# Performance work log

Hardware: AMD Instinct MI355X
Metric: run time of the kernel (lower is better)

The kernel has to match this reference:

```python
import jax, jax.numpy as jnp
import numpy as np
import math

B, S, HID = 2, 2048, 1024
D = 64            # size_per_head
H = HID // D      # num heads = 16
ROT = 32          # rotary_hsize = size_per_head // 2


def _apply_rotary(qk, sinusoids):
    # qk: [B, S, H, D]; sinusoids: [B, 2, S, ROT]
    sin = sinusoids[:, 0, :, None, :]   # [B, S, 1, ROT]
    cos = sinusoids[:, 1, :, None, :]
    qk_rope = qk[..., :ROT]
    # torch.stack([-a[..., ::2], a[..., 1::2]], -1).reshape(a.shape)
    rot2 = jnp.stack([-qk_rope[..., ::2], qk_rope[..., 1::2]], axis=-1).reshape(qk_rope.shape)
    qk_rope = qk_rope * cos + rot2 * sin
    return jnp.concatenate([qk_rope, qk[..., ROT:]], axis=-1)


def setup_inputs() -> dict:
    key = jax.random.key(0)
    ks = jax.random.split(key, 8)
    sc = 1.0 / math.sqrt(HID)
    return {
        "x": jax.random.normal(ks[0], (B, S, HID), jnp.float32),
        "sinusoids": jax.random.normal(ks[1], (B, 2, S, ROT), jnp.float32),
        "attention_bias": jax.random.uniform(ks[2], (B, 1, S, S), jnp.float32),
        "Wq": jax.random.normal(ks[3], (HID, HID), jnp.float32) * sc,
        "bq": jnp.zeros((HID,), jnp.float32),
        "Wk": jax.random.normal(ks[4], (HID, HID), jnp.float32) * sc,
        "bk": jnp.zeros((HID,), jnp.float32),
        "Wv": jax.random.normal(ks[5], (HID, HID), jnp.float32) * sc,
        "bv": jnp.zeros((HID,), jnp.float32),
        "Wo": jax.random.normal(ks[6], (HID, HID), jnp.float32) * sc,
    }


def reference(x, sinusoids, attention_bias, Wq, bq, Wk, bk, Wv, bv, Wo):
    q = (x @ Wq + bq).reshape(B, S, H, D)
    k = (x @ Wk + bk).reshape(B, S, H, D)
    v = (x @ Wv + bv).reshape(B, S, H, D)
    # original concatenates q,k along the heads dim before rotary; since rotary
    # broadcasts over heads, applying it to each separately is identical math
    q = _apply_rotary(q, sinusoids)
    k = _apply_rotary(k, sinusoids)
    q = q / math.sqrt(D)
    scores = jnp.einsum('bqhd,bkhd->bhqk', q, k)          # [B,H,S,S]
    probs = jax.nn.softmax(scores, axis=-1)
    probs = probs * attention_bias                         # multiplicative bias AFTER softmax
    out = jnp.einsum('bhqk,bkhd->bqhd', probs, v)          # [B,S,H,D]
    out = out.reshape(B, S, HID)
    return out @ Wo
```

## Files before the change

kernel.cpp:

```cpp
#include <hip/hip_runtime.h>
#include <math.h>

#define B_   2
#define S_   2048
#define HID_ 1024
#define D_   64
#define H_   16
#define ROT_ 32
#define M_   (B_*S_)

typedef __attribute__((ext_vector_type(4))) short  short4v;
typedef __attribute__((ext_vector_type(8))) short  short8;
typedef __attribute__((ext_vector_type(4))) float  floatx4;
typedef __attribute__((ext_vector_type(16))) float floatx16;
typedef __attribute__((ext_vector_type(2))) unsigned int uint2v;

__device__ __forceinline__ unsigned short f2bf(float f) {
  unsigned int x = __builtin_bit_cast(unsigned int, f);
  x += 0x7fffu + ((x >> 16) & 1u);
  return (unsigned short)(x >> 16);
}
__device__ __forceinline__ unsigned int cvt_pk_bf16(float lo, float hi) {
  unsigned int r;
  asm("v_cvt_pk_bf16_f32 %0, %1, %2" : "=v"(r) : "v"(lo), "v"(hi));
  return r;
}
__device__ __forceinline__ void gload_lds16(const unsigned short* g, unsigned short* l) {
  __builtin_amdgcn_global_load_lds(
      (const __attribute__((address_space(1))) unsigned int*)g,
      (__attribute__((address_space(3))) unsigned int*)l, 16, 0, 0);
}

__global__ void cast_bf16(const float* __restrict__ in, unsigned short* __restrict__ out) {
  int i = (blockIdx.x * 256 + threadIdx.x) * 4;
  floatx4 v = *(const floatx4*)(in + i);
  unsigned short o[4];
  o[0] = f2bf(v[0]); o[1] = f2bf(v[1]); o[2] = f2bf(v[2]); o[3] = f2bf(v[3]);
  *(unsigned long long*)(out + i) = *(unsigned long long*)o;
}

__global__ void transW(const float* __restrict__ W0, const float* __restrict__ W1,
                       const float* __restrict__ W2, const float* __restrict__ W3,
                       unsigned short* __restrict__ T0, unsigned short* __restrict__ T1,
                       unsigned short* __restrict__ T2, unsigned short* __restrict__ T3) {
  const float* W; unsigned short* T;
  int z = blockIdx.z;
  if (z == 0)      { W = W0; T = T0; }
  else if (z == 1) { W = W1; T = T1; }
  else if (z == 2) { W = W2; T = T2; }
  else             { W = W3; T = T3; }
  __shared__ float tile[32][33];
  int bx = blockIdx.x * 32, by = blockIdx.y * 32;
  int tx = threadIdx.x, ty = threadIdx.y;
  #pragma unroll
  for (int j = 0; j < 4; j++)
    tile[ty + j*8][tx] = W[(size_t)(by + ty + j*8) * HID_ + bx + tx];
  __syncthreads();
  #pragma unroll
  for (int j = 0; j < 4; j++)
    T[(size_t)(bx + ty + j*8) * HID_ + by + tx] = f2bf(tile[tx][ty + j*8]);
}

template <int MODE>
__global__ __launch_bounds__(256) void gemm_bt(
    const unsigned short* __restrict__ A,
    const unsigned short* __restrict__ Bt0, const unsigned short* __restrict__ Bt1,
    const unsigned short* __restrict__ Bt2,
    const float* __restrict__ bias0, const float* __restrict__ bias1,
    const float* __restrict__ bias2,
    void* __restrict__ out0, void* __restrict__ out1, void* __restrict__ out2,
    const float* __restrict__ sins, float sc0)
{
  const unsigned short* Bt; const float* bias; void* Out; float sc;
  if (blockIdx.z == 0)      { Bt = Bt0; bias = bias0; Out = out0; sc = sc0; }
  else if (blockIdx.z == 1) { Bt = Bt1; bias = bias1; Out = out1; sc = 1.f; }
  else                      { Bt = Bt2; bias = bias2; Out = out2; sc = 1.f; }
  const int K = HID_, N = HID_;
  int m0 = blockIdx.y * 128, n0 = blockIdx.x * 128;
  __shared__ alignas(16) unsigned short sA[128 * 32];
  __shared__ alignas(16) unsigned short sB[128 * 32];
  int t = threadIdx.x;
  int lane = t & 63, wave = t >> 6;
  int quad = lane >> 4, l16 = lane & 15;
  int wr = wave >> 1, wc = wave & 1;

  int srow = (lane >> 2), scol = (lane & 3) * 8;
  const unsigned short* gA0 = A  + (size_t)(m0 + wave*32 +  0 + srow) * K + scol;
  const unsigned short* gA1 = A  + (size_t)(m0 + wave*32 + 16 + srow) * K + scol;
  const unsigned short* gB0 = Bt + (size_t)(n0 + wave*32 +  0 + srow) * K + scol;
  const unsigned short* gB1 = Bt + (size_t)(n0 + wave*32 + 16 + srow) * K + scol;
  unsigned short* lA0 = sA + (wave*32 +  0) * 32;
  unsigned short* lA1 = sA + (wave*32 + 16) * 32;
  unsigned short* lB0 = sB + (wave*32 +  0) * 32;
  unsigned short* lB1 = sB + (wave*32 + 16) * 32;

  floatx4 acc[4][4];
  #pragma unroll
  for (int i = 0; i < 4; i++)
    #pragma unroll
    for (int j = 0; j < 4; j++)
      acc[i][j] = (floatx4){0.f, 0.f, 0.f, 0.f};

  for (int k0 = 0; k0 < K; k0 += 32) {
    gload_lds16(gA0 + k0, lA0);
    gload_lds16(gA1 + k0, lA1);
    gload_lds16(gB0 + k0, lB0);
    gload_lds16(gB1 + k0, lB1);
    __syncthreads();
    short8 af[4], bf[4];
    #pragma unroll
    for (int i = 0; i < 4; i++) {
      af[i] = *(const short8*)(sA + (wr * 64 + i * 16 + l16) * 32 + quad * 8);
      bf[i] = *(const short8*)(sB + (wc * 64 + i * 16 + l16) * 32 + quad * 8);
    }
    #pragma unroll
    for (int i = 0; i < 4; i++)
      #pragma unroll
      for (int j = 0; j < 4; j++)
        acc[i][j] = __builtin_amdgcn_mfma_f32_16x16x32_bf16(af[i], bf[j], acc[i][j], 0, 0, 0);
    __syncthreads();
  }

  #pragma unroll
  for (int i = 0; i < 4; i++) {
    int mbase = m0 + wr * 64 + i * 16 + quad * 4;
    #pragma unroll
    for (int j = 0; j < 4; j++) {
      int n = n0 + wc * 64 + j * 16 + l16;
      float bv = bias ? bias[n] : 0.f;
      if (MODE == 1) {
        #pragma unroll
        for (int r = 0; r < 4; r++)
          ((float*)Out)[(size_t)(mbase + r) * N + n] = acc[i][j][r] + bv;
      } else if (blockIdx.z == 2) {
        int bb = mbase >> 11, ss = mbase & 2047;
        int hh = n >> 6, dd = n & 63;
        unsigned short pk[4];
        #pragma unroll
        for (int r = 0; r < 4; r++) pk[r] = f2bf(acc[i][j][r] + bv);
        *(unsigned long long*)((unsigned short*)Out +
            (((size_t)(bb * H_ + hh) * D_ + dd) * S_ + ss)) = *(unsigned long long*)pk;
      } else if (j < 2) {
        int jh = j * 16 + l16;
        #pragma unroll
        for (int r = 0; r < 4; r++) {
          int row = mbase + r, bb = row >> 11, ss = row & 2047;
          float sn = sins[((size_t)(bb * 2 + 0) * S_ + ss) * ROT_ + jh];
          float cs = sins[((size_t)(bb * 2 + 1) * S_ + ss) * ROT_ + jh];
          float f = (jh & 1) ? (cs + sn) : (cs - sn);
          ((unsigned short*)Out)[(size_t)row * N + n] = f2bf((acc[i][j][r] + bv) * f * sc);
        }
      } else {
        #pragma unroll
        for (int r = 0; r < 4; r++)
          ((unsigned short*)Out)[(size_t)(mbase + r) * N + n] = f2bf((acc[i][j][r] + bv) * sc);
      }
    }
  }
}

__global__ __launch_bounds__(256) void gemm_bt64(
    const unsigned short* __restrict__ A, const unsigned short* __restrict__ Bt,
    float* __restrict__ Out)
{
  const int K = HID_, N = HID_;
  int m0 = blockIdx.y * 128, n0 = blockIdx.x * 64;
  __shared__ alignas(16) unsigned short sA[128 * 32];
  __shared__ alignas(16) unsigned short sB[64 * 32];
  int t = threadIdx.x;
  int lane = t & 63, wave = t >> 6;
  int quad = lane >> 4, l16 = lane & 15;
  int wr = wave >> 1, wc = wave & 1;

  int srow = lane >> 2, scol = (lane & 3) * 8;
  const unsigned short* gA0 = A  + (size_t)(m0 + wave*32 +  0 + srow) * K + scol;
  const unsigned short* gA1 = A  + (size_t)(m0 + wave*32 + 16 + srow) * K + scol;
  const unsigned short* gB0 = Bt + (size_t)(n0 + wave*16 + srow) * K + scol;
  unsigned short* lA0 = sA + (wave*32 +  0) * 32;
  unsigned short* lA1 = sA + (wave*32 + 16) * 32;
  unsigned short* lB0 = sB + (wave*16) * 32;

  floatx4 acc[4][2];
  #pragma unroll
  for (int i = 0; i < 4; i++)
    #pragma unroll
    for (int j = 0; j < 2; j++)
      acc[i][j] = (floatx4){0.f, 0.f, 0.f, 0.f};

  for (int k0 = 0; k0 < K; k0 += 32) {
    gload_lds16(gA0 + k0, lA0);
    gload_lds16(gA1 + k0, lA1);
    gload_lds16(gB0 + k0, lB0);
    __syncthreads();
    short8 af[4], bf[2];
    #pragma unroll
    for (int i = 0; i < 4; i++)
      af[i] = *(const short8*)(sA + (wr * 64 + i * 16 + l16) * 32 + quad * 8);
    #pragma unroll
    for (int j = 0; j < 2; j++)
      bf[j] = *(const short8*)(sB + (wc * 32 + j * 16 + l16) * 32 + quad * 8);
    #pragma unroll
    for (int i = 0; i < 4; i++)
      #pragma unroll
      for (int j = 0; j < 2; j++)
        acc[i][j] = __builtin_amdgcn_mfma_f32_16x16x32_bf16(af[i], bf[j], acc[i][j], 0, 0, 0);
    __syncthreads();
  }

  #pragma unroll
  for (int i = 0; i < 4; i++) {
    int mbase = m0 + wr * 64 + i * 16 + quad * 4;
    #pragma unroll
    for (int j = 0; j < 2; j++) {
      int n = n0 + wc * 32 + j * 16 + l16;
      #pragma unroll
      for (int r = 0; r < 4; r++)
        Out[(size_t)(mbase + r) * N + n] = acc[i][j][r];
    }
  }
}

__global__ __launch_bounds__(512, 2) void attn(
    const unsigned short* __restrict__ Q, const unsigned short* __restrict__ Kb,
    const unsigned short* __restrict__ Vt, const float* __restrict__ bias,
    unsigned short* __restrict__ Out)
{
  int b = blockIdx.z, h = blockIdx.y;
  int t = threadIdx.x;
  int lane = t & 63, wave = t >> 6;
  int g = wave >> 2, wg = wave & 3;
  int l32 = lane & 31, hl = lane >> 5;
  int q0 = blockIdx.x * 128 + wg * 32;
  const int RS = H_ * D_;
  const int NT = S_ / 128;

  __shared__ alignas(16) unsigned short smem[2 * 18432];
  unsigned short* sKg = smem + g * 18432;
  unsigned short* sVg = sKg + 9216;

  const unsigned short* Qbase = Q + ((size_t)(b * S_) * H_ + h) * D_;
  const unsigned short* Kbase = Kb + ((size_t)(b * S_) * H_ + h) * D_;
  const unsigned short* Vbase = Vt + ((size_t)(b * H_) + h) * D_ * S_;

  short8 qf[4];
  {
    const unsigned short* qp = Qbase + (size_t)(q0 + l32) * RS + 8 * hl;
    qf[0] = *(const short8*)(qp);
    qf[1] = *(const short8*)(qp + 16);
    qf[2] = *(const short8*)(qp + 32);
    qf[3] = *(const short8*)(qp + 48);
  }

  int tg = t & 255;
  int srow = tg >> 2, sq = tg & 3;
  const unsigned short* gK = Kbase + (size_t)(g * 1024 + srow) * RS + sq * 16;
  const unsigned short* gV = Vbase + (size_t)srow * S_ + g * 1024 + sq * 16;
  const int wOff = srow * 72 + sq * 16;

  const float* bp = bias + (size_t)b * S_ * S_ + (size_t)(q0 + l32) * S_ + g * 1024 + 4 * hl;

  float l_run = 0.f;
  floatx16 o0, o1;
  #pragma unroll
  for (int r = 0; r < 16; r++) { o0[r] = 0.f; o1[r] = 0.f; }

  floatx4 kp[2], vp[2];
  kp[0] = *(const floatx4*)(gK);     kp[1] = *(const floatx4*)(gK + 8);
  vp[0] = *(const floatx4*)(gV);     vp[1] = *(const floatx4*)(gV + 8);
  *(floatx4*)(sKg + wOff)     = kp[0];
  *(floatx4*)(sKg + wOff + 8) = kp[1];
  *(floatx4*)(sVg + wOff)     = vp[0];
  *(floatx4*)(sVg + wOff + 8) = vp[1];
  kp[0] = *(const floatx4*)(gK + (size_t)64 * RS);
  kp[1] = *(const floatx4*)(gK + (size_t)64 * RS + 8);
  vp[0] = *(const floatx4*)(gV + 64);
  vp[1] = *(const floatx4*)(gV + 64 + 8);

  for (int it = 0; it < NT; ++it) {
    int cur = it & 1, nxt = cur ^ 1;
    __syncthreads();

    if (it < NT - 1) {
      *(floatx4*)(sKg + nxt * 4608 + wOff)     = kp[0];
      *(floatx4*)(sKg + nxt * 4608 + wOff + 8) = kp[1];
      *(floatx4*)(sVg + nxt * 4608 + wOff)     = vp[0];
      *(floatx4*)(sVg + nxt * 4608 + wOff + 8) = vp[1];
    }
    {
      int k2 = ((it + 2) & (NT - 1)) * 64;
      kp[0] = *(const floatx4*)(gK + (size_t)k2 * RS);
      kp[1] = *(const floatx4*)(gK + (size_t)k2 * RS + 8);
      vp[0] = *(const floatx4*)(gV + k2);
      vp[1] = *(const floatx4*)(gV + k2 + 8);
    }

    floatx4 bl[8];
    #pragma unroll
    for (int cc = 0; cc < 2; cc++)
      #pragma unroll
      for (int rg = 0; rg < 4; rg++)
        bl[cc * 4 + rg] = *(const floatx4*)(bp + it * 64 + cc * 32 + 8 * rg);

    const unsigned short* sKc = sKg + cur * 4608;
    const unsigned short* sVc = sVg + cur * 4608;

    floatx16 st[2];
    __builtin_amdgcn_s_setprio(1);
    #pragma unroll
    for (int cc = 0; cc < 2; cc++) {
      floatx16 s;
      #pragma unroll
      for (int r = 0; r < 16; r++) s[r] = 0.f;
      #pragma unroll
      for (int ks = 0; ks < 4; ks++) {
        short8 kf = *(const short8*)(sKc + (cc * 32 + l32) * 72 + 16 * ks + 8 * hl);
        s = __builtin_amdgcn_mfma_f32_32x32x16_bf16(kf, qf[ks], s, 0, 0, 0);
      }
      st[cc] = s;
    }
    __builtin_amdgcn_s_setprio(0);

    short4v pf[2][4];
    #pragma unroll
    for (int cc = 0; cc < 2; cc++)
      #pragma unroll
      for (int rg = 0; rg < 4; rg++) {
        float p0 = __builtin_amdgcn_exp2f(st[cc][rg * 4 + 0]);
        float p1 = __builtin_amdgcn_exp2f(st[cc][rg * 4 + 1]);
        float p2 = __builtin_amdgcn_exp2f(st[cc][rg * 4 + 2]);
        float p3 = __builtin_amdgcn_exp2f(st[cc][rg * 4 + 3]);
        l_run += (p0 + p1) + (p2 + p3);
        uint2v u;
        u[0] = cvt_pk_bf16(p0 * bl[cc * 4 + rg][0], p1 * bl[cc * 4 + rg][1]);
        u[1] = cvt_pk_bf16(p2 * bl[cc * 4 + rg][2], p3 * bl[cc * 4 + rg][3]);
        pf[cc][rg] = __builtin_bit_cast(short4v, u);
      }

    __builtin_amdgcn_s_setprio(1);
    #pragma unroll
    for (int cc = 0; cc < 2; cc++)
      #pragma unroll
      for (int gg = 0; gg < 4; gg++) {
        int kcol = cc * 32 + 8 * gg + 4 * hl;
        short4v vf0 = *(const short4v*)(sVc + (l32)      * 72 + kcol);
        short4v vf1 = *(const short4v*)(sVc + (32 + l32) * 72 + kcol);
        o0 = __builtin_amdgcn_mfma_f32_32x32x8bf16_1k(pf[cc][gg], vf0, o0, 0, 0, 0);
        o1 = __builtin_amdgcn_mfma_f32_32x32x8bf16_1k(pf[cc][gg], vf1, o1, 0, 0, 0);
      }
    __builtin_amdgcn_s_setprio(0);
  }

  float l2 = l_run + __shfl_xor(l_run, 32);

  float* sO = (float*)(smem + 18432);
  float* sL = sO + 128 * 64;

  __syncthreads();
  if (g == 1) {
    #pragma unroll
    for (int r = 0; r < 16; r++) {
      int ql = (r & 3) + 8 * (r >> 2) + 4 * hl;
      sO[(wg * 32 + ql) * 64 + l32]      = o0[r];
      sO[(wg * 32 + ql) * 64 + 32 + l32] = o1[r];
    }
    if (hl == 0) sL[wg * 32 + l32] = l2;
  }
  __syncthreads();
  if (g == 0) {
    float linv = __builtin_amdgcn_rcpf(l2 + sL[wg * 32 + l32]);
    #pragma unroll
    for (int r = 0; r < 16; r++) {
      int ql = (r & 3) + 8 * (r >> 2) + 4 * hl;
      float sc = __shfl(linv, ql);
      size_t base = ((size_t)(b * S_ + q0 + ql) * H_ + h) * D_;
      float a0 = o0[r] + sO[(wg * 32 + ql) * 64 + l32];
      float a1 = o1[r] + sO[(wg * 32 + ql) * 64 + 32 + l32];
      Out[base + l32]      = f2bf(a0 * sc);
      Out[base + 32 + l32] = f2bf(a1 * sc);
    }
  }
}

extern "C" void kernel_launch(void* const* d_in, const int* in_sizes, int n_in,
                              void* d_out, int out_size, void* d_ws, size_t ws_size,
                              hipStream_t stream) {
  (void)in_sizes; (void)n_in; (void)out_size; (void)ws_size;
  const float* x    = (const float*)d_in[0];
  const float* sins = (const float*)d_in[1];
  const float* ab   = (const float*)d_in[2];
  const float* Wq   = (const float*)d_in[3];
  const float* bq   = (const float*)d_in[4];
  const float* Wk   = (const float*)d_in[5];
  const float* bk   = (const float*)d_in[6];
  const float* Wv   = (const float*)d_in[7];
  const float* bv   = (const float*)d_in[8];
  const float* Wo   = (const float*)d_in[9];
  float* out = (float*)d_out;
  char* ws = (char*)d_ws;

  unsigned short* xb  = (unsigned short*)(ws);
  unsigned short* Wqt = (unsigned short*)(ws + ((size_t) 8 << 20));
  unsigned short* Wkt = (unsigned short*)(ws + ((size_t)10 << 20));
  unsigned short* Wvt = (unsigned short*)(ws + ((size_t)12 << 20));
  unsigned short* Wot = (unsigned short*)(ws + ((size_t)14 << 20));
  unsigned short* Qb  = (unsigned short*)(ws + ((size_t)16 << 20));
  unsigned short* Kb  = (unsigned short*)(ws + ((size_t)24 << 20));
  unsigned short* Vtb = (unsigned short*)(ws + ((size_t)32 << 20));
  unsigned short* Ab  = (unsigned short*)(ws + ((size_t)40 << 20));

  const float c1 = 0.125f * 1.44269504088896f;

  cast_bf16<<<dim3((M_ * HID_) / (256 * 4)), dim3(256), 0, stream>>>(x, xb);
  transW<<<dim3(32, 32, 4), dim3(32, 8), 0, stream>>>(Wq, Wk, Wv, Wo, Wqt, Wkt, Wvt, Wot);
  gemm_bt<0><<<dim3(8, 32, 3), dim3(256), 0, stream>>>(xb, Wqt, Wkt, Wvt, bq, bk, bv,
                                                       Qb, Kb, Vtb, sins, c1);
  attn<<<dim3(S_ / 128, H_, B_), dim3(512), 0, stream>>>(Qb, Kb, Vtb, ab, Ab);
  gemm_bt64<<<dim3(HID_ / 64, M_ / 128), dim3(256), 0, stream>>>(Ab, Wot, out);
}
```

Before: 284.9 us.

## Use direct global-to-LDS loads with XOR swizzle and interleave score/PV MFMA halves

Replaces the register-staged K/V prefetch with direct global-to-LDS async loads (gload_lds16) into a double buffer whose columns are XOR-swizzled instead of padded to a stride of 72. The 64-key tile is split into two 32-key halves so that the QK^T MFMAs for the second half overlap the softmax and PV MFMAs of the first. Bias loads for the next tile are issued early to hide their latency. This cuts register pressure and LDS padding, at the cost of relying on the gload_lds16 helper and the swizzle being correct, and it changes the shared-memory layout used in the epilogue.

```diff
diff --git a/kernel.cpp b/kernel.cpp
--- a/kernel.cpp
+++ b/kernel.cpp
@@ -230,13 +230,13 @@
   int lane = t & 63, wave = t >> 6;
   int g = wave >> 2, wg = wave & 3;
   int l32 = lane & 31, hl = lane >> 5;
+  int s7 = l32 & 7;
   int q0 = blockIdx.x * 128 + wg * 32;
   const int RS = H_ * D_;
   const int NT = S_ / 128;
 
-  __shared__ alignas(16) unsigned short smem[2 * 18432];
-  unsigned short* sKg = smem + g * 18432;
-  unsigned short* sVg = sKg + 9216;
+  __shared__ alignas(16) unsigned short smem[32768];
+  unsigned short* bg = smem + g * 16384;
 
   const unsigned short* Qbase = Q + ((size_t)(b * S_) * H_ + h) * D_;
   const unsigned short* Kbase = Kb + ((size_t)(b * S_) * H_ + h) * D_;
@@ -252,108 +252,128 @@
   }
 
   int tg = t & 255;
-  int srow = tg >> 2, sq = tg & 3;
-  const unsigned short* gK = Kbase + (size_t)(g * 1024 + srow) * RS + sq * 16;
-  const unsigned short* gV = Vbase + (size_t)srow * S_ + g * 1024 + sq * 16;
-  const int wOff = srow * 72 + sq * 16;
+  int row0 = tg >> 3;
+  int csw  = (tg & 7) ^ (row0 & 7);
+  const unsigned short* gK0 = Kbase + (size_t)(g*1024 + row0)      * RS + csw * 8;
+  const unsigned short* gK1 = Kbase + (size_t)(g*1024 + row0 + 32) * RS + csw * 8;
+  const unsigned short* gV0 = Vbase + (size_t)(row0)      * S_ + g*1024 + csw * 8;
+  const unsigned short* gV1 = Vbase + (size_t)(row0 + 32) * S_ + g*1024 + csw * 8;
 
   const float* bp = bias + (size_t)b * S_ * S_ + (size_t)(q0 + l32) * S_ + g * 1024 + 4 * hl;
+
+#define STAGE(bi, tk) do { \
+    unsigned short* kb_ = bg + (bi) * 4096; \
+    unsigned short* vb_ = bg + 8192 + (bi) * 4096; \
+    size_t ko_ = (size_t)(tk) * 64 * RS; int vo_ = (tk) * 64; \
+    gload_lds16(gK0 + ko_, kb_ + tg * 8); \
+    gload_lds16(gK1 + ko_, kb_ + (256 + tg) * 8); \
+    gload_lds16(gV0 + vo_, vb_ + tg * 8); \
+    gload_lds16(gV1 + vo_, vb_ + (256 + tg) * 8); \
+  } while (0)
 
   float l_run = 0.f;
   floatx16 o0, o1;
   #pragma unroll
   for (int r = 0; r < 16; r++) { o0[r] = 0.f; o1[r] = 0.f; }
 
-  floatx4 kp[2], vp[2];
-  kp[0] = *(const floatx4*)(gK);     kp[1] = *(const floatx4*)(gK + 8);
-  vp[0] = *(const floatx4*)(gV);     vp[1] = *(const floatx4*)(gV + 8);
-  *(floatx4*)(sKg + wOff)     = kp[0];
-  *(floatx4*)(sKg + wOff + 8) = kp[1];
-  *(floatx4*)(sVg + wOff)     = vp[0];
-  *(floatx4*)(sVg + wOff + 8) = vp[1];
-  kp[0] = *(const floatx4*)(gK + (size_t)64 * RS);
-  kp[1] = *(const floatx4*)(gK + (size_t)64 * RS + 8);
-  vp[0] = *(const floatx4*)(gV + 64);
-  vp[1] = *(const floatx4*)(gV + 64 + 8);
+  STAGE(0, 0);
+  floatx4 b0[4], b1[4];
+  #pragma unroll
+  for (int rg = 0; rg < 4; rg++) {
+    b0[rg] = *(const floatx4*)(bp + 8 * rg);
+    b1[rg] = *(const floatx4*)(bp + 32 + 8 * rg);
+  }
 
   for (int it = 0; it < NT; ++it) {
-    int cur = it & 1, nxt = cur ^ 1;
+    int cur = it & 1;
     __syncthreads();
-
-    if (it < NT - 1) {
-      *(floatx4*)(sKg + nxt * 4608 + wOff)     = kp[0];
-      *(floatx4*)(sKg + nxt * 4608 + wOff + 8) = kp[1];
-      *(floatx4*)(sVg + nxt * 4608 + wOff)     = vp[0];
-      *(floatx4*)(sVg + nxt * 4608 + wOff + 8) = vp[1];
-    }
-    {
-      int k2 = ((it + 2) & (NT - 1)) * 64;
-      kp[0] = *(const floatx4*)(gK + (size_t)k2 * RS);
-      kp[1] = *(const floatx4*)(gK + (size_t)k2 * RS + 8);
-      vp[0] = *(const floatx4*)(gV + k2);
-      vp[1] = *(const floatx4*)(gV + k2 + 8);
-    }
-
-    floatx4 bl[8];
-    #pragma unroll
-    for (int cc = 0; cc < 2; cc++)
-      #pragma unroll
-      for (int rg = 0; rg < 4; rg++)
-        bl[cc * 4 + rg] = *(const floatx4*)(bp + it * 64 + cc * 32 + 8 * rg);
-
-    const unsigned short* sKc = sKg + cur * 4608;
-    const unsigned short* sVc = sVg + cur * 4608;
-
-    floatx16 st[2];
+    if (it < NT - 1) STAGE(cur ^ 1, it + 1);
+
+    const unsigned short* kbuf = bg + cur * 4096;
+    const unsigned short* vbuf = bg + 8192 + cur * 4096;
+    int itn = ((it + 1) & (NT - 1)) * 64;
+
+    floatx16 st;
+    #pragma unroll
+    for (int r = 0; r < 16; r++) st[r] = 0.f;
     __builtin_amdgcn_s_setprio(1);
     #pragma unroll
-    for (int cc = 0; cc < 2; cc++) {
-      floatx16 s;
-      #pragma unroll
-      for (int r = 0; r < 16; r++) s[r] = 0.f;
-      #pragma unroll
-      for (int ks = 0; ks < 4; ks++) {
-        short8 kf = *(const short8*)(sKc + (cc * 32 + l32) * 72 + 16 * ks + 8 * hl);
-        s = __builtin_amdgcn_mfma_f32_32x32x16_bf16(kf, qf[ks], s, 0, 0, 0);
-      }
-      st[cc] = s;
+    for (int ks = 0; ks < 4; ks++) {
+      short8 kf = *(const short8*)(kbuf + l32 * 64 + (((2 * ks + hl) ^ s7) * 8));
+      st = __builtin_amdgcn_mfma_f32_32x32x16_bf16(kf, qf[ks], st, 0, 0, 0);
     }
     __builtin_amdgcn_s_setprio(0);
 
-    short4v pf[2][4];
-    #pragma unroll
-    for (int cc = 0; cc < 2; cc++)
-      #pragma unroll
-      for (int rg = 0; rg < 4; rg++) {
-        float p0 = __builtin_amdgcn_exp2f(st[cc][rg * 4 + 0]);
-        float p1 = __builtin_amdgcn_exp2f(st[cc][rg * 4 + 1]);
-        float p2 = __builtin_amdgcn_exp2f(st[cc][rg * 4 + 2]);
-        float p3 = __builtin_amdgcn_exp2f(st[cc][rg * 4 + 3]);
-        l_run += (p0 + p1) + (p2 + p3);
-        uint2v u;
-        u[0] = cvt_pk_bf16(p0 * bl[cc * 4 + rg][0], p1 * bl[cc * 4 + rg][1]);
-        u[1] = cvt_pk_bf16(p2 * bl[cc * 4 + rg][2], p3 * bl[cc * 4 + rg][3]);
-        pf[cc][rg] = __builtin_bit_cast(short4v, u);
-      }
-
+    short4v pf0[4];
+    #pragma unroll
+    for (int rg = 0; rg < 4; rg++) {
+      float p0 = __builtin_amdgcn_exp2f(st[rg * 4 + 0]);
+      float p1 = __builtin_amdgcn_exp2f(st[rg * 4 + 1]);
+      float p2 = __builtin_amdgcn_exp2f(st[rg * 4 + 2]);
+      float p3 = __builtin_amdgcn_exp2f(st[rg * 4 + 3]);
+      l_run += (p0 + p1) + (p2 + p3);
+      uint2v u;
+      u[0] = cvt_pk_bf16(p0 * b0[rg][0], p1 * b0[rg][1]);
+      u[1] = cvt_pk_bf16(p2 * b0[rg][2], p3 * b0[rg][3]);
+      pf0[rg] = __builtin_bit_cast(short4v, u);
+    }
+    #pragma unroll
+    for (int rg = 0; rg < 4; rg++)
+      b0[rg] = *(const floatx4*)(bp + itn + 8 * rg);
+
+    floatx16 st1;
+    #pragma unroll
+    for (int r = 0; r < 16; r++) st1[r] = 0.f;
     __builtin_amdgcn_s_setprio(1);
     #pragma unroll
-    for (int cc = 0; cc < 2; cc++)
-      #pragma unroll
-      for (int gg = 0; gg < 4; gg++) {
-        int kcol = cc * 32 + 8 * gg + 4 * hl;
-        short4v vf0 = *(const short4v*)(sVc + (l32)      * 72 + kcol);
-        short4v vf1 = *(const short4v*)(sVc + (32 + l32) * 72 + kcol);
-        o0 = __builtin_amdgcn_mfma_f32_32x32x8bf16_1k(pf[cc][gg], vf0, o0, 0, 0, 0);
-        o1 = __builtin_amdgcn_mfma_f32_32x32x8bf16_1k(pf[cc][gg], vf1, o1, 0, 0, 0);
-      }
+    for (int ks = 0; ks < 4; ks++) {
+      short8 kf = *(const short8*)(kbuf + (32 + l32) * 64 + (((2 * ks + hl) ^ s7) * 8));
+      st1 = __builtin_amdgcn_mfma_f32_32x32x16_bf16(kf, qf[ks], st1, 0, 0, 0);
+    }
+    #pragma unroll
+    for (int gg = 0; gg < 4; gg++) {
+      int ch = (gg ^ s7) * 8 + hl * 4;
+      short4v vf0 = *(const short4v*)(vbuf + l32 * 64 + ch);
+      short4v vf1 = *(const short4v*)(vbuf + (32 + l32) * 64 + ch);
+      o0 = __builtin_amdgcn_mfma_f32_32x32x8bf16_1k(pf0[gg], vf0, o0, 0, 0, 0);
+      o1 = __builtin_amdgcn_mfma_f32_32x32x8bf16_1k(pf0[gg], vf1, o1, 0, 0, 0);
+    }
     __builtin_amdgcn_s_setprio(0);
-  }
+
+    short4v pf1[4];
+    #pragma unroll
+    for (int rg = 0; rg < 4; rg++) {
+      float p0 = __builtin_amdgcn_exp2f(st1[rg * 4 + 0]);
+      float p1 = __builtin_amdgcn_exp2f(st1[rg * 4 + 1]);
+      float p2 = __builtin_amdgcn_exp2f(st1[rg * 4 + 2]);
+      float p3 = __builtin_amdgcn_exp2f(st1[rg * 4 + 3]);
+      l_run += (p0 + p1) + (p2 + p3);
+      uint2v u;
+      u[0] = cvt_pk_bf16(p0 * b1[rg][0], p1 * b1[rg][1]);
+      u[1] = cvt_pk_bf16(p2 * b1[rg][2], p3 * b1[rg][3]);
+      pf1[rg] = __builtin_bit_cast(short4v, u);
+    }
+    #pragma unroll
+    for (int rg = 0; rg < 4; rg++)
+      b1[rg] = *(const floatx4*)(bp + itn + 32 + 8 * rg);
+
+    __builtin_amdgcn_s_setprio(1);
+    #pragma unroll
+    for (int gg = 0; gg < 4; gg++) {
+      int ch = ((4 + gg) ^ s7) * 8 + hl * 4;
+      short4v vf0 = *(const short4v*)(vbuf + l32 * 64 + ch);
+      short4v vf1 = *(const short4v*)(vbuf + (32 + l32) * 64 + ch);
+      o0 = __builtin_amdgcn_mfma_f32_32x32x8bf16_1k(pf1[gg], vf0, o0, 0, 0, 0);
+      o1 = __builtin_amdgcn_mfma_f32_32x32x8bf16_1k(pf1[gg], vf1, o1, 0, 0, 0);
+    }
+    __builtin_amdgcn_s_setprio(0);
+  }
+#undef STAGE
 
   float l2 = l_run + __shfl_xor(l_run, 32);
 
-  float* sO = (float*)(smem + 18432);
-  float* sL = sO + 128 * 64;
+  float* sO = (float*)smem;
+  float* sL = (float*)(smem + 16384);
 
   __syncthreads();
   if (g == 1) {
```

After: 277.7 us. -2.5%, faster.
